# Performance work log

Measured on AMD Instinct MI355X. Metric: run time of the kernel, lower is better.

## Reference

```python
import jax, jax.numpy as jnp
import numpy as np

N = 100000
E = 3200000
IN_C = 128
HID = [32, 32]
OUT_C = 32
NEG_SLOPE = 0.2  # PyG GATConv default leaky_relu slope


def setup_inputs() -> dict:
    key = jax.random.key(0)
    ks = jax.random.split(key, 16)
    x = jax.random.normal(ks[0], (N, IN_C), dtype=jnp.float32)
    edge_index = jax.random.randint(ks[1], (2, E), 0, N, dtype=jnp.int32)

    def glorot(k, shape):
        fan_in, fan_out = shape[0], shape[-1]
        lim = jnp.sqrt(6.0 / (fan_in + fan_out))
        return jax.random.uniform(k, shape, jnp.float32, -lim, lim)

    # GAT layer 1: 128 -> 32, heads=1
    W1 = glorot(ks[2], (IN_C, HID[0]))
    a_src1 = glorot(ks[3], (HID[0],))
    a_dst1 = glorot(ks[4], (HID[0],))
    b1 = jnp.zeros((HID[0],), jnp.float32)
    # GAT layer 2: 32 -> 32
    W2 = glorot(ks[5], (HID[0], HID[1]))
    a_src2 = glorot(ks[6], (HID[1],))
    a_dst2 = glorot(ks[7], (HID[1],))
    b2 = jnp.zeros((HID[1],), jnp.float32)
    # classifier: 32 -> 32
    Wc = glorot(ks[8], (HID[1], OUT_C))
    bc = jnp.zeros((OUT_C,), jnp.float32)
    return {"x": x, "edge_index": edge_index,
            "W1": W1, "a_src1": a_src1, "a_dst1": a_dst1, "b1": b1,
            "W2": W2, "a_src2": a_src2, "a_dst2": a_dst2, "b2": b2,
            "Wc": Wc, "bc": bc}


def gat_conv(h_in, src, dst, W, a_src, a_dst, b, n_nodes):
    """PyG GATConv with heads=1: linear, per-edge leaky-relu score,
    segment-softmax over incoming edges of dst, weighted scatter-sum."""
    h = h_in @ W                                   # [N, C]
    s_src = h @ a_src                              # [N]
    s_dst = h @ a_dst                              # [N]
    e = jax.nn.leaky_relu(s_src[src] + s_dst[dst], NEG_SLOPE)  # [E']
    m = jax.ops.segment_max(e, dst, num_segments=n_nodes)
    m = jnp.where(jnp.isfinite(m), m, 0.0)
    ex = jnp.exp(e - m[dst])
    z = jax.ops.segment_sum(ex, dst, num_segments=n_nodes)
    alpha = ex / (z[dst] + 1e-16)                  # [E']
    out = jax.ops.segment_sum(alpha[:, None] * h[src], dst, num_segments=n_nodes)
    return out + b


def reference(x, edge_index, W1, a_src1, a_dst1, b1, W2, a_src2, a_dst2, b2, Wc, bc):
    n = x.shape[0]
    # PyG GATConv default add_self_loops=True
    loop = jnp.arange(n, dtype=edge_index.dtype)
    src = jnp.concatenate([edge_index[0], loop])
    dst = jnp.concatenate([edge_index[1], loop])
    h = jax.nn.relu(gat_conv(x, src, dst, W1, a_src1, a_dst1, b1, n))
    h = jax.nn.relu(gat_conv(h, src, dst, W2, a_src2, a_dst2, b2, n))
    logits = h @ Wc + bc
    return jax.nn.sigmoid(logits)
```

## Files before the change

### kernel.cpp

```cpp
#include <hip/hip_runtime.h>
#include <hip/hip_fp16.h>
#include <math.h>

#define NS 0.2f

__device__ __forceinline__ float lrelu(float x) { return fmaxf(x, NS * x); }


__global__ __launch_bounds__(256) void k_feat1(
    const float* __restrict__ X, const float* __restrict__ W,
    const float* __restrict__ a_s, const float* __restrict__ a_d,
    __half* __restrict__ H, float* __restrict__ Ss, float* __restrict__ Sd, int n)
{
    __shared__ float Wl[128 * 32];
    __shared__ float Xl[8 * 128];
    const int tid = threadIdx.x;
    for (int i = tid; i < 128 * 32; i += 256) Wl[i] = W[i];

    const int row0 = blockIdx.x * 8;
    {
        int idx = tid * 4;
        int r = idx >> 7, c = idx & 127;
        if (row0 + r < n)
            *reinterpret_cast<float4*>(&Xl[idx]) =
                *reinterpret_cast<const float4*>(&X[(size_t)(row0 + r) * 128 + c]);
    }
    __syncthreads();

    const int r = tid >> 5, c = tid & 31;
    const int row = row0 + r;
    if (row >= n) return;

    float acc = 0.f;
#pragma unroll
    for (int k = 0; k < 128; ++k) acc += Xl[r * 128 + k] * Wl[k * 32 + c];
    H[(size_t)row * 32 + c] = __float2half(acc);

    float vs = acc * a_s[c];
    float vd = acc * a_d[c];
#pragma unroll
    for (int o = 16; o; o >>= 1) { vs += __shfl_xor(vs, o, 32); vd += __shfl_xor(vd, o, 32); }
    if (c == 0) { Ss[row] = vs; Sd[row] = vd; }
}

__global__ __launch_bounds__(256) void k_feat2(
    const float* __restrict__ In, const float* __restrict__ W,
    const float* __restrict__ bias,
    const float* __restrict__ a_s, const float* __restrict__ a_d,
    __half* __restrict__ H, float* __restrict__ Ss, float* __restrict__ Sd, int n)
{
    __shared__ float Wl[32 * 32];
    __shared__ float Xl[8 * 32];
    const int tid = threadIdx.x;
    for (int i = tid; i < 1024; i += 256) Wl[i] = W[i];

    const int r = tid >> 5, c = tid & 31;
    const int row = blockIdx.x * 8 + r;
    if (row < n) Xl[tid] = fmaxf(In[(size_t)row * 32 + c] + bias[c], 0.f);
    __syncthreads();
    if (row >= n) return;

    float acc = 0.f;
#pragma unroll
    for (int k = 0; k < 32; ++k) acc += Xl[r * 32 + k] * Wl[k * 32 + c];
    H[(size_t)row * 32 + c] = __float2half(acc);

    float vs = acc * a_s[c];
    float vd = acc * a_d[c];
#pragma unroll
    for (int o = 16; o; o >>= 1) { vs += __shfl_xor(vs, o, 32); vd += __shfl_xor(vd, o, 32); }
    if (c == 0) { Ss[row] = vs; Sd[row] = vd; }
}

__global__ __launch_bounds__(256) void k_cls(
    const float* __restrict__ In, const float* __restrict__ W,
    const float* __restrict__ b_prev, const float* __restrict__ bc,
    float* __restrict__ Out, int n)
{
    __shared__ float Wl[32 * 32];
    __shared__ float Xl[8 * 32];
    const int tid = threadIdx.x;
    for (int i = tid; i < 1024; i += 256) Wl[i] = W[i];

    const int r = tid >> 5, c = tid & 31;
    const int row = blockIdx.x * 8 + r;
    if (row < n) Xl[tid] = fmaxf(In[(size_t)row * 32 + c] + b_prev[c], 0.f);
    __syncthreads();
    if (row >= n) return;

    float acc = bc[c];
#pragma unroll
    for (int k = 0; k < 32; ++k) acc += Xl[r * 32 + k] * Wl[k * 32 + c];
    Out[(size_t)row * 32 + c] = 1.f / (1.f + __expf(-acc));
}


#define NBH 256
#define BPAD 32

__global__ __launch_bounds__(256) void k_bhist(const int* __restrict__ edst, int E,
                                               int* __restrict__ hpart, int ngroups)
{
    __shared__ int h[512];
    const int tid = threadIdx.x;
    for (int i = tid; i < ngroups; i += 256) h[i] = 0;
    __syncthreads();
    const int nv = E >> 2;
    for (int i = blockIdx.x * 256 + tid; i < nv; i += NBH * 256) {
        int4 d = *reinterpret_cast<const int4*>(&edst[i << 2]);
        atomicAdd(&h[d.x >> 8], 1); atomicAdd(&h[d.y >> 8], 1);
        atomicAdd(&h[d.z >> 8], 1); atomicAdd(&h[d.w >> 8], 1);
    }
    if (blockIdx.x == 0 && tid < (E & 3))
        atomicAdd(&h[edst[(nv << 2) + tid] >> 8], 1);
    __syncthreads();
    for (int i = tid; i < ngroups; i += 256) hpart[i * NBH + blockIdx.x] = h[i];
}

__global__ __launch_bounds__(512) void k_bscan(const int* __restrict__ hpart, int ngroups,
    int* __restrict__ bstart, int* __restrict__ bcur, int* __restrict__ off,
    int N, int E)
{
    __shared__ int sm[512];
    int t = threadIdx.x;
    int v = 0;
    if (t < ngroups) {
        const int4* row = reinterpret_cast<const int4*>(&hpart[t * NBH]);
#pragma unroll 4
        for (int b = 0; b < NBH / 4; ++b) { int4 x = row[b]; v += x.x + x.y + x.z + x.w; }
    }
    sm[t] = v; __syncthreads();
    for (int o = 1; o < 512; o <<= 1) {
        int x = sm[t];
        if (t >= o) x += sm[t - o];
        __syncthreads();
        sm[t] = x;
        __syncthreads();
    }
    if (t <= ngroups) {
        int ex = (t == 0) ? 0 : sm[t - 1];
        bstart[t] = ex;
        if (t < ngroups) bcur[t * BPAD] = ex;
    }
    if (t == 0) off[N] = E + N;
}

#define CHUNK 4096
#define KPT 8

__global__ __launch_bounds__(512) void k_part(
    const int* __restrict__ esrc, const int* __restrict__ edst, int E,
    int* __restrict__ bcur, unsigned int* __restrict__ ebuf, int ngroups)
{
    __shared__ int hist[512];
    __shared__ int lofs[513];
    __shared__ int gbase[512];
    __shared__ unsigned int stage[CHUNK];
    __shared__ unsigned short bstage[CHUNK];
    const int tid = threadIdx.x;

    for (int c0 = blockIdx.x * CHUNK; c0 < E; c0 += gridDim.x * CHUNK) {
        const int cnt = min(CHUNK, E - c0);
        if (tid < 512) hist[tid] = 0;
        __syncthreads();

        int bp[KPT];
#pragma unroll
        for (int k = 0; k < KPT; ++k) {
            int i = c0 + k * 512 + tid;
            bp[k] = -1;
            if (i < E) {
                int d = edst[i];
                int b = d >> 8;
                int pos = atomicAdd(&hist[b], 1);
                bp[k] = (b << 20) | ((d & 255) << 12) | pos;
            }
        }
        __syncthreads();

        if (tid < 64) {
            int base = tid * 8, v[8], s = 0;
#pragma unroll
            for (int k = 0; k < 8; ++k) { v[k] = hist[base + k]; s += v[k]; }
            int pre = s;
            for (int o = 1; o < 64; o <<= 1) {
                int t2 = __shfl_up(pre, o, 64);
                if (tid >= o) pre += t2;
            }
            pre -= s;
#pragma unroll
            for (int k = 0; k < 8; ++k) { lofs[base + k] = pre; pre += v[k]; }
            if (tid == 63) lofs[512] = pre;
        }
        __syncthreads();

        for (int b = tid; b < ngroups; b += 512)
            if (hist[b] > 0) gbase[b] = atomicAdd(&bcur[b * BPAD], hist[b]);
        __syncthreads();

#pragma unroll
        for (int k = 0; k < KPT; ++k) {
            if (bp[k] >= 0) {
                int i = c0 + k * 512 + tid;
                int b = bp[k] >> 20, dl = (bp[k] >> 12) & 255, pos = bp[k] & 4095;
                int slot = lofs[b] + pos;
                stage[slot] = ((unsigned)dl << 24) | (unsigned)esrc[i];
                bstage[slot] = (unsigned short)b;
            }
        }
        __syncthreads();

        for (int i = tid; i < cnt; i += 512) {
            int b = bstage[i];
            ebuf[(size_t)gbase[b] + (i - lofs[b])] = stage[i];
        }
        __syncthreads();
    }
}

#define RCAP 11264

__global__ __launch_bounds__(256) void k_place2(
    const unsigned int* __restrict__ ebuf, const int* __restrict__ bstart,
    int* __restrict__ off, int* __restrict__ esorted, int* __restrict__ gcur, int N)
{
    __shared__ int R[RCAP];
    __shared__ int cnt[256];
    __shared__ int lcur[256];
    __shared__ int sm[256];
    const int g = blockIdx.x, tid = threadIdx.x;
    const int d0 = g << 8, d1 = min(d0 + 256, N);
    const int nd = d1 - d0;
    const int eb = bstart[g];
    const int ecnt = bstart[g + 1] - eb;
    const int base = eb + d0;
    const int len = ecnt + nd;

    cnt[tid] = 0;
    __syncthreads();
    for (int i = tid; i < ecnt; i += 256)
        atomicAdd(&cnt[ebuf[eb + i] >> 24], 1);
    __syncthreads();

    int v = (tid < nd) ? cnt[tid] + 1 : 0;
    sm[tid] = v; __syncthreads();
    for (int o = 1; o < 256; o <<= 1) {
        int x = sm[tid];
        if (tid >= o) x += sm[tid - o];
        __syncthreads();
        sm[tid] = x;
        __syncthreads();
    }
    int lo = sm[tid] - v;

    if (len <= RCAP) {
        if (tid < nd) {
            off[d0 + tid] = base + lo;
            R[lo] = d0 + tid;
            lcur[tid] = lo + 1;
        }
        __syncthreads();
        for (int i = tid; i < ecnt; i += 256) {
            unsigned int w = ebuf[eb + i];
            int pos = atomicAdd(&lcur[w >> 24], 1);
            R[pos] = (int)(w & 0xffffffu);
        }
        __syncthreads();
        for (int i = tid; i < len; i += 256) esorted[base + i] = R[i];
    } else {
        if (tid < nd) {
            off[d0 + tid] = base + lo;
            esorted[base + lo] = d0 + tid;
            gcur[d0 + tid] = base + lo + 1;
        }
        __syncthreads();
        for (int i = tid; i < ecnt; i += 256) {
            unsigned int w = ebuf[eb + i];
            esorted[atomicAdd(&gcur[d0 + (int)(w >> 24)], 1)] = (int)(w & 0xffffffu);
        }
    }
}


__global__ __launch_bounds__(256) void k_gat(
    const int* __restrict__ off, const int* __restrict__ esorted,
    const float* __restrict__ Ss, const float* __restrict__ Sd,
    const uint4* __restrict__ H4, float* __restrict__ out, int n)
{
    const int g = blockIdx.x * 4 + (threadIdx.x >> 6);
    if (g >= n) return;
    const int lane = threadIdx.x & 63;
    const int hf = lane & 3, q = lane >> 2;

    const float sd = Sd[g];
    const int j0 = off[g], j1 = off[g + 1];

    float a0 = 0.f, a1 = 0.f, a2 = 0.f, a3 = 0.f;
    float a4 = 0.f, a5 = 0.f, a6 = 0.f, a7 = 0.f, z = 0.f;

    for (int b0 = j0; b0 < j1; b0 += 64) {
        int e = b0 + lane;
        int sAll = 0; float wAll = 0.f;
        if (e < j1) {
            sAll = esorted[e];
            float t = Ss[sAll] + sd;
            wAll = __expf(fmaxf(t, NS * t));
        }
        z += wAll;
        const int m = min(64, j1 - b0);
        for (int k = 0; k < m; k += 32) {
            int   s0 = __shfl(sAll, k + q);
            float w0 = __shfl(wAll, k + q);
            int   s1 = __shfl(sAll, k + 16 + q);
            float w1 = __shfl(wAll, k + 16 + q);
            uint4 h0 = {0, 0, 0, 0};
            uint4 h1 = {0, 0, 0, 0};
            if (k + q < m)      h0 = H4[(size_t)s0 * 4 + hf];
            if (k + 16 + q < m) h1 = H4[(size_t)s1 * 4 + hf];
            {
                float2 f0 = __half22float2(*reinterpret_cast<const __half2*>(&h0.x));
                float2 f1 = __half22float2(*reinterpret_cast<const __half2*>(&h0.y));
                float2 f2 = __half22float2(*reinterpret_cast<const __half2*>(&h0.z));
                float2 f3 = __half22float2(*reinterpret_cast<const __half2*>(&h0.w));
                a0 += w0 * f0.x; a1 += w0 * f0.y;
                a2 += w0 * f1.x; a3 += w0 * f1.y;
                a4 += w0 * f2.x; a5 += w0 * f2.y;
                a6 += w0 * f3.x; a7 += w0 * f3.y;
            }
            {
                float2 f0 = __half22float2(*reinterpret_cast<const __half2*>(&h1.x));
                float2 f1 = __half22float2(*reinterpret_cast<const __half2*>(&h1.y));
                float2 f2 = __half22float2(*reinterpret_cast<const __half2*>(&h1.z));
                float2 f3 = __half22float2(*reinterpret_cast<const __half2*>(&h1.w));
                a0 += w1 * f0.x; a1 += w1 * f0.y;
                a2 += w1 * f1.x; a3 += w1 * f1.y;
                a4 += w1 * f2.x; a5 += w1 * f2.y;
                a6 += w1 * f3.x; a7 += w1 * f3.y;
            }
        }
    }

#pragma unroll
    for (int o = 4; o <= 32; o <<= 1) {
        a0 += __shfl_xor(a0, o); a1 += __shfl_xor(a1, o);
        a2 += __shfl_xor(a2, o); a3 += __shfl_xor(a3, o);
        a4 += __shfl_xor(a4, o); a5 += __shfl_xor(a5, o);
        a6 += __shfl_xor(a6, o); a7 += __shfl_xor(a7, o);
        z  += __shfl_xor(z, o);
    }
    z += __shfl_xor(z, 1);
    z += __shfl_xor(z, 2);

    if (q == 0) {
        float inv = 1.f / (z + 1e-16f);
        float4 r0 = { a0 * inv, a1 * inv, a2 * inv, a3 * inv };
        float4 r1 = { a4 * inv, a5 * inv, a6 * inv, a7 * inv };
        float* o32 = &out[(size_t)g * 32 + hf * 8];
        *reinterpret_cast<float4*>(o32)     = r0;
        *reinterpret_cast<float4*>(o32 + 4) = r1;
    }
}


extern "C" void kernel_launch(void* const* d_in, const int* in_sizes, int n_in,
                              void* d_out, int out_size, void* d_ws, size_t ws_size,
                              hipStream_t stream)
{
    const float* x   = (const float*)d_in[0];
    const int*   ei  = (const int*)d_in[1];
    const float* W1  = (const float*)d_in[2];
    const float* as1 = (const float*)d_in[3];
    const float* ad1 = (const float*)d_in[4];
    const float* b1  = (const float*)d_in[5];
    const float* W2  = (const float*)d_in[6];
    const float* as2 = (const float*)d_in[7];
    const float* ad2 = (const float*)d_in[8];
    const float* b2  = (const float*)d_in[9];
    const float* Wc  = (const float*)d_in[10];
    const float* bc  = (const float*)d_in[11];

    const int N = in_sizes[0] / 128;
    const int E = in_sizes[1] / 2;
    const int* esrc = ei;
    const int* edst = ei + E;
    const int ngroups = (N + 255) >> 8;

    char* p = (char*)d_ws;
    __half* H    = (__half*)p; p += (size_t)N * 32 * 2;
    float* AGG   = (float*)p;  p += (size_t)N * 32 * 4;
    float* Ss    = (float*)p;  p += (size_t)N * 4;
    float* Sd    = (float*)p;  p += (size_t)N * 4;
    int*   off   = (int*)p;    p += (size_t)(N + 1) * 4;
    int*   gcur  = (int*)p;    p += (size_t)N * 4;
    int*   hpart = (int*)p;    p += 512 * NBH * 4;
    int*   bstart= (int*)p;    p += 513 * 4;
    int*   bcur  = (int*)p;    p += 512 * BPAD * 4;
    int*   esort = (int*)p;    p += (size_t)(E + N) * 4;

    unsigned int* ebuf = (unsigned int*)H;
    const uint4* H4 = (const uint4*)H;

    const dim3 blk(256);
    const int nb_rows = (N + 7) / 8;
    const int nb_part = (E + CHUNK - 1) / CHUNK;

    k_bhist<<<NBH, blk, 0, stream>>>(edst, E, hpart, ngroups);
    k_bscan<<<1, 512, 0, stream>>>(hpart, ngroups, bstart, bcur, off, N, E);
    k_part<<<nb_part, 512, 0, stream>>>(esrc, edst, E, bcur, ebuf, ngroups);
    k_place2<<<ngroups, blk, 0, stream>>>(ebuf, bstart, off, esort, gcur, N);

    k_feat1<<<nb_rows, blk, 0, stream>>>(x, W1, as1, ad1, H, Ss, Sd, N);
    k_gat<<<(N + 3) / 4, blk, 0, stream>>>(off, esort, Ss, Sd, H4, AGG, N);

    k_feat2<<<nb_rows, blk, 0, stream>>>(AGG, W2, b1, as2, ad2, H, Ss, Sd, N);
    k_gat<<<(N + 3) / 4, blk, 0, stream>>>(off, esort, Ss, Sd, H4, AGG, N);

    k_cls<<<nb_rows, blk, 0, stream>>>(AGG, Wc, b2, bc, (float*)d_out, N);
}
```

Before: 262.5 us.

## Process two destination nodes per wavefront with batched first-chunk gathers

Each wavefront now handles two consecutive destination nodes. For both nodes it loads the first 64 edges and issues up to eight independent 16-byte feature gathers before accumulating, which raises memory-level parallelism. Average degree is about 33, so most nodes fit entirely in this first chunk. Any remaining edges go through a per-node tail loop. The change roughly doubles accumulator registers, which may lower occupancy, and it halves the grid size.

```diff
diff --git a/kernel.cpp b/kernel.cpp
--- a/kernel.cpp
+++ b/kernel.cpp
@@ -287,77 +287,149 @@
     const float* __restrict__ Ss, const float* __restrict__ Sd,
     const uint4* __restrict__ H4, float* __restrict__ out, int n)
 {
-    const int g = blockIdx.x * 4 + (threadIdx.x >> 6);
-    if (g >= n) return;
+    const int gA = (blockIdx.x * 4 + (threadIdx.x >> 6)) * 2;
+    if (gA >= n) return;
+    const int gB = gA + 1;
+    const bool hasB = (gB < n);
     const int lane = threadIdx.x & 63;
     const int hf = lane & 3, q = lane >> 2;
 
-    const float sd = Sd[g];
-    const int j0 = off[g], j1 = off[g + 1];
-
-    float a0 = 0.f, a1 = 0.f, a2 = 0.f, a3 = 0.f;
-    float a4 = 0.f, a5 = 0.f, a6 = 0.f, a7 = 0.f, z = 0.f;
-
-    for (int b0 = j0; b0 < j1; b0 += 64) {
+    const int j0A = off[gA], j1A = off[gA + 1];
+    const int j0B = hasB ? j1A : 0, j1B = hasB ? off[gB + 1] : 0;
+    const float sdA = Sd[gA];
+    const float sdB = hasB ? Sd[gB] : 0.f;
+
+    int eA = j0A + lane, eB = j0B + lane;
+    int rA = (eA < j1A) ? esorted[eA] : -1;
+    int rB = (eB < j1B) ? esorted[eB] : -1;
+    float ssA = (rA >= 0) ? Ss[rA] : 0.f;
+    float ssB = (rB >= 0) ? Ss[rB] : 0.f;
+    int   sA = (rA >= 0) ? rA : 0;
+    int   sB = (rB >= 0) ? rB : 0;
+    float wA = 0.f, wB = 0.f;
+    if (rA >= 0) { float t = ssA + sdA; wA = __expf(fmaxf(t, NS * t)); }
+    if (rB >= 0) { float t = ssB + sdB; wB = __expf(fmaxf(t, NS * t)); }
+    float zA = wA, zB = wB;
+
+    const int mA = min(64, j1A - j0A);
+    const int mB = min(64, j1B - j0B);
+
+    float accA[8] = {0.f,0.f,0.f,0.f,0.f,0.f,0.f,0.f};
+    float accB[8] = {0.f,0.f,0.f,0.f,0.f,0.f,0.f,0.f};
+
+    {
+        int   sAk[4], sBk[4];
+        float wAk[4], wBk[4];
+        uint4 hA[4], hB[4];
+#pragma unroll
+        for (int i = 0; i < 4; ++i) {
+            sAk[i] = __shfl(sA, i * 16 + q);
+            wAk[i] = __shfl(wA, i * 16 + q);
+            hA[i] = make_uint4(0u, 0u, 0u, 0u);
+            if (i * 16 + q < mA) hA[i] = H4[(size_t)sAk[i] * 4 + hf];
+        }
+#pragma unroll
+        for (int i = 0; i < 4; ++i) {
+            sBk[i] = __shfl(sB, i * 16 + q);
+            wBk[i] = __shfl(wB, i * 16 + q);
+            hB[i] = make_uint4(0u, 0u, 0u, 0u);
+            if (i * 16 + q < mB) hB[i] = H4[(size_t)sBk[i] * 4 + hf];
+        }
+#pragma unroll
+        for (int i = 0; i < 4; ++i) {
+            float w = wAk[i];
+            const __half2* hp = reinterpret_cast<const __half2*>(&hA[i]);
+#pragma unroll
+            for (int j = 0; j < 4; ++j) {
+                float2 f = __half22float2(hp[j]);
+                accA[j * 2]     += w * f.x;
+                accA[j * 2 + 1] += w * f.y;
+            }
+        }
+#pragma unroll
+        for (int i = 0; i < 4; ++i) {
+            float w = wBk[i];
+            const __half2* hp = reinterpret_cast<const __half2*>(&hB[i]);
+#pragma unroll
+            for (int j = 0; j < 4; ++j) {
+                float2 f = __half22float2(hp[j]);
+                accB[j * 2]     += w * f.x;
+                accB[j * 2 + 1] += w * f.y;
+            }
+        }
+    }
+
+    for (int b0 = j0A + 64; b0 < j1A; b0 += 64) {
         int e = b0 + lane;
-        int sAll = 0; float wAll = 0.f;
-        if (e < j1) {
-            sAll = esorted[e];
-            float t = Ss[sAll] + sd;
-            wAll = __expf(fmaxf(t, NS * t));
-        }
-        z += wAll;
-        const int m = min(64, j1 - b0);
-        for (int k = 0; k < m; k += 32) {
-            int   s0 = __shfl(sAll, k + q);
-            float w0 = __shfl(wAll, k + q);
-            int   s1 = __shfl(sAll, k + 16 + q);
-            float w1 = __shfl(wAll, k + 16 + q);
-            uint4 h0 = {0, 0, 0, 0};
-            uint4 h1 = {0, 0, 0, 0};
-            if (k + q < m)      h0 = H4[(size_t)s0 * 4 + hf];
-            if (k + 16 + q < m) h1 = H4[(size_t)s1 * 4 + hf];
-            {
-                float2 f0 = __half22float2(*reinterpret_cast<const __half2*>(&h0.x));
-                float2 f1 = __half22float2(*reinterpret_cast<const __half2*>(&h0.y));
-                float2 f2 = __half22float2(*reinterpret_cast<const __half2*>(&h0.z));
-                float2 f3 = __half22float2(*reinterpret_cast<const __half2*>(&h0.w));
-                a0 += w0 * f0.x; a1 += w0 * f0.y;
-                a2 += w0 * f1.x; a3 += w0 * f1.y;
-                a4 += w0 * f2.x; a5 += w0 * f2.y;
-                a6 += w0 * f3.x; a7 += w0 * f3.y;
-            }
-            {
-                float2 f0 = __half22float2(*reinterpret_cast<const __half2*>(&h1.x));
-                float2 f1 = __half22float2(*reinterpret_cast<const __half2*>(&h1.y));
-                float2 f2 = __half22float2(*reinterpret_cast<const __half2*>(&h1.z));
-                float2 f3 = __half22float2(*reinterpret_cast<const __half2*>(&h1.w));
-                a0 += w1 * f0.x; a1 += w1 * f0.y;
-                a2 += w1 * f1.x; a3 += w1 * f1.y;
-                a4 += w1 * f2.x; a5 += w1 * f2.y;
-                a6 += w1 * f3.x; a7 += w1 * f3.y;
+        int sT = 0; float wT = 0.f;
+        if (e < j1A) { sT = esorted[e]; float t = Ss[sT] + sdA; wT = __expf(fmaxf(t, NS * t)); }
+        zA += wT;
+        const int m = min(64, j1A - b0);
+        for (int k = 0; k < m; k += 16) {
+            int   src = __shfl(sT, k + q);
+            float w   = __shfl(wT, k + q);
+            if (k + q < m) {
+                uint4 hv = H4[(size_t)src * 4 + hf];
+                const __half2* hp = reinterpret_cast<const __half2*>(&hv);
+#pragma unroll
+                for (int j = 0; j < 4; ++j) {
+                    float2 f = __half22float2(hp[j]);
+                    accA[j * 2]     += w * f.x;
+                    accA[j * 2 + 1] += w * f.y;
+                }
+            }
+        }
+    }
+    for (int b0 = j0B + 64; b0 < j1B; b0 += 64) {
+        int e = b0 + lane;
+        int sT = 0; float wT = 0.f;
+        if (e < j1B) { sT = esorted[e]; float t = Ss[sT] + sdB; wT = __expf(fmaxf(t, NS * t)); }
+        zB += wT;
+        const int m = min(64, j1B - b0);
+        for (int k = 0; k < m; k += 16) {
+            int   src = __shfl(sT, k + q);
+            float w   = __shfl(wT, k + q);
+            if (k + q < m) {
+                uint4 hv = H4[(size_t)src * 4 + hf];
+                const __half2* hp = reinterpret_cast<const __half2*>(&hv);
+#pragma unroll
+                for (int j = 0; j < 4; ++j) {
+                    float2 f = __half22float2(hp[j]);
+                    accB[j * 2]     += w * f.x;
+                    accB[j * 2 + 1] += w * f.y;
+                }
             }
         }
     }
 
 #pragma unroll
     for (int o = 4; o <= 32; o <<= 1) {
-        a0 += __shfl_xor(a0, o); a1 += __shfl_xor(a1, o);
-        a2 += __shfl_xor(a2, o); a3 += __shfl_xor(a3, o);
-        a4 += __shfl_xor(a4, o); a5 += __shfl_xor(a5, o);
-        a6 += __shfl_xor(a6, o); a7 += __shfl_xor(a7, o);
-        z  += __shfl_xor(z, o);
-    }
-    z += __shfl_xor(z, 1);
-    z += __shfl_xor(z, 2);
+#pragma unroll
+        for (int j = 0; j < 8; ++j) {
+            accA[j] += __shfl_xor(accA[j], o);
+            accB[j] += __shfl_xor(accB[j], o);
+        }
+        zA += __shfl_xor(zA, o);
+        zB += __shfl_xor(zB, o);
+    }
+    zA += __shfl_xor(zA, 1); zA += __shfl_xor(zA, 2);
+    zB += __shfl_xor(zB, 1); zB += __shfl_xor(zB, 2);
 
     if (q == 0) {
-        float inv = 1.f / (z + 1e-16f);
-        float4 r0 = { a0 * inv, a1 * inv, a2 * inv, a3 * inv };
-        float4 r1 = { a4 * inv, a5 * inv, a6 * inv, a7 * inv };
-        float* o32 = &out[(size_t)g * 32 + hf * 8];
+        float invA = 1.f / (zA + 1e-16f);
+        float4 r0 = { accA[0] * invA, accA[1] * invA, accA[2] * invA, accA[3] * invA };
+        float4 r1 = { accA[4] * invA, accA[5] * invA, accA[6] * invA, accA[7] * invA };
+        float* o32 = &out[(size_t)gA * 32 + hf * 8];
         *reinterpret_cast<float4*>(o32)     = r0;
         *reinterpret_cast<float4*>(o32 + 4) = r1;
+        if (hasB) {
+            float invB = 1.f / (zB + 1e-16f);
+            float4 r2 = { accB[0] * invB, accB[1] * invB, accB[2] * invB, accB[3] * invB };
+            float4 r3 = { accB[4] * invB, accB[5] * invB, accB[6] * invB, accB[7] * invB };
+            float* p32 = &out[(size_t)gB * 32 + hf * 8];
+            *reinterpret_cast<float4*>(p32)     = r2;
+            *reinterpret_cast<float4*>(p32 + 4) = r3;
+        }
     }
 }
 
@@ -403,6 +475,7 @@
     const dim3 blk(256);
     const int nb_rows = (N + 7) / 8;
     const int nb_part = (E + CHUNK - 1) / CHUNK;
+    const int nb_gat  = (N + 7) / 8;
 
     k_bhist<<<NBH, blk, 0, stream>>>(edst, E, hpart, ngroups);
     k_bscan<<<1, 512, 0, stream>>>(hpart, ngroups, bstart, bcur, off, N, E);
@@ -410,10 +483,10 @@
     k_place2<<<ngroups, blk, 0, stream>>>(ebuf, bstart, off, esort, gcur, N);
 
     k_feat1<<<nb_rows, blk, 0, stream>>>(x, W1, as1, ad1, H, Ss, Sd, N);
-    k_gat<<<(N + 3) / 4, blk, 0, stream>>>(off, esort, Ss, Sd, H4, AGG, N);
+    k_gat<<<nb_gat, blk, 0, stream>>>(off, esort, Ss, Sd, H4, AGG, N);
 
     k_feat2<<<nb_rows, blk, 0, stream>>>(AGG, W2, b1, as2, ad2, H, Ss, Sd, N);
-    k_gat<<<(N + 3) / 4, blk, 0, stream>>>(off, esort, Ss, Sd, H4, AGG, N);
+    k_gat<<<nb_gat, blk, 0, stream>>>(off, esort, Ss, Sd, H4, AGG, N);
 
     k_cls<<<nb_rows, blk, 0, stream>>>(AGG, Wc, b2, bc, (float*)d_out, N);
 }
```

Result: no change. 263.1 us (+0.3%).
